# Kernel optimization log

Hardware: AMD Instinct MI355X
Metric: run time of the kernel (lower is better)

## Reference

```python
import jax, jax.numpy as jnp
import numpy as np
from functools import partial

H = 50  # hidden size hardcoded in the module


def _lstm_cell(x, h, c, W_ih, W_hh, b_ih, b_hh):
    # PyTorch LSTMCell math, gate order i, f, g, o
    gates = x @ W_ih.T + h @ W_hh.T + b_ih + b_hh  # [B, 4H]
    i, f, g, o = jnp.split(gates, 4, axis=-1)
    c_new = jax.nn.sigmoid(f) * c + jax.nn.sigmoid(i) * jnp.tanh(g)
    h_new = jax.nn.sigmoid(o) * jnp.tanh(c_new)
    return h_new, c_new


def setup_inputs() -> dict:
    key = jax.random.key(0)
    ks = jax.random.split(key, 11)
    B, T = 512, 1024

    def w(k, shape, fan_in):
        return (jax.random.normal(k, shape, jnp.float32) / np.sqrt(fan_in)).astype(jnp.float32)

    return {
        "x": jax.random.normal(ks[0], (B, T), jnp.float32),
        "W_ih1": w(ks[1], (4 * H, 1), H),
        "W_hh1": w(ks[2], (4 * H, H), H),
        "b_ih1": w(ks[3], (4 * H,), H),
        "b_hh1": w(ks[4], (4 * H,), H),
        "W_ih2": w(ks[5], (4 * H, H), H),
        "W_hh2": w(ks[6], (4 * H, H), H),
        "b_ih2": w(ks[7], (4 * H,), H),
        "b_hh2": w(ks[8], (4 * H,), H),
        "W_lin": w(ks[9], (1, H), H),
        "b_lin": w(ks[10], (1,), H),
        "predict": 32,
    }


def reference(x, W_ih1, W_hh1, b_ih1, b_hh1, W_ih2, W_hh2, b_ih2, b_hh2,
              W_lin, b_lin, predict):
    B = x.shape[0]
    z = jnp.zeros((B, H), x.dtype)
    init = (z, z, z, z)

    def step(carry, x_t):  # x_t: [B, 1]
        h1, c1, h2, c2 = carry
        h1, c1 = _lstm_cell(x_t, h1, c1, W_ih1, W_hh1, b_ih1, b_hh1)
        h2, c2 = _lstm_cell(h1, h2, c2, W_ih2, W_hh2, b_ih2, b_hh2)
        out = h2 @ W_lin.T + b_lin  # [B, 1]
        return (h1, c1, h2, c2), out

    xs = jnp.swapaxes(x, 0, 1)[:, :, None]  # [T, B, 1]
    carry, outs = jax.lax.scan(step, init, xs)  # outs: [T, B, 1]

    if predict > 0:
        h1, c1, h2, c2 = carry

        def pstep(pcarry, _):
            h1, c1, h2, c2, o = pcarry
            h1, c1 = _lstm_cell(o, h1, c1, W_ih1, W_hh1, b_ih1, b_hh1)
            h2, c2 = _lstm_cell(h1, h2, c2, W_ih2, W_hh2, b_ih2, b_hh2)
            out = h2 @ W_lin.T + b_lin
            return (h1, c1, h2, c2, out), out

        _, pouts = jax.lax.scan(pstep, (h1, c1, h2, c2, outs[-1]), None, length=predict)
        outs = jnp.concatenate([outs, pouts], axis=0)

    # stack(dim=1).squeeze(2) -> [B, T + predict]
    return jnp.swapaxes(outs[..., 0], 0, 1)
```

## Files before the change

### kernel.cpp

```cpp
#include <hip/hip_runtime.h>


#define Hh   50
#define TLEN 1024

typedef _Float16 half2v __attribute__((ext_vector_type(2)));

#if __has_builtin(__builtin_amdgcn_fdot2)
#define FDOT2(a, b, c) __builtin_amdgcn_fdot2((a), (b), (c), false)
#else
#define FDOT2(a, b, c) ((c) + (float)(a)[0] * (float)(b)[0] + (float)(a)[1] * (float)(b)[1])
#endif

#define BC(f) __builtin_bit_cast(half2v, f)

__device__ __forceinline__ float fast_sigmoid(float v) {
    return 1.0f / (1.0f + __expf(-v));
}
__device__ __forceinline__ float fast_tanh(float v) {
    return 1.0f - 2.0f / (__expf(2.0f * v) + 1.0f);
}
__device__ __forceinline__ void lds_fence() {
    asm volatile("" ::: "memory");
    __builtin_amdgcn_sched_barrier(0);
}

#define SHADOW(CARRY, BUF, SLOT) do {                                        \
    _Pragma("unroll")                                                        \
    for (int L_ = 0; L_ < 6; ++L_) {                                         \
        float4 f_ = *(const float4*)&BUF[SLOT][8 * L_];                      \
        CARRY[4*L_] = f_.x; CARRY[4*L_+1] = f_.y;                            \
        CARRY[4*L_+2] = f_.z; CARRY[4*L_+3] = f_.w;                          \
    }                                                                        \
    CARRY[24] = *(const float*)&BUF[SLOT][48];                               \
} while (0)

extern "C" __global__ __launch_bounds__(128, 1)
void sine_lstm_kernel(const float* __restrict__ x,
                      const float* __restrict__ W_ih1,
                      const float* __restrict__ W_hh1,
                      const float* __restrict__ b_ih1,
                      const float* __restrict__ b_hh1,
                      const float* __restrict__ W_ih2,
                      const float* __restrict__ W_hh2,
                      const float* __restrict__ b_ih2,
                      const float* __restrict__ b_hh2,
                      const float* __restrict__ W_lin,
                      const float* __restrict__ b_lin,
                      const int*   __restrict__ predict_p,
                      float* __restrict__ out,
                      int T)
{
    __shared__ __align__(16) float    x_lds[TLEN];
    __shared__ __align__(16) _Float16 h1lds[2][64];
    __shared__ __align__(16) _Float16 h2lds[2][64];
    __shared__ __align__(16) float    h2f32[2][64];
    __shared__ __align__(16) float    part[2][4][64][4];

    const int tid = threadIdx.x;
    const int wv  = tid >> 6;
    const int ln  = tid & 63;
    const bool isProd = (wv == 0);
    const int b   = blockIdx.x;
    const int predict = *predict_p;
    const int S = T + predict;

    for (int i = tid; i < TLEN; i += 128)
        x_lds[i] = x[(size_t)b * T + i];
    ((_Float16*)h1lds)[tid] = (_Float16)0.0f;
    ((_Float16*)h2lds)[tid] = (_Float16)0.0f;
    ((float*)h2f32)[tid] = 0.0f;

    const bool act = (ln < Hh);

    const float* MA = isProd ? W_hh1 : W_hh2;
    const int    pbase = isProd ? 0 : 12;
    half2v wgtA[4][25], wgtB[4][13];
    float  b1v[4], b2v[4], wih[4];
    #pragma unroll
    for (int q = 0; q < 4; ++q) {
        const int r = act ? (q * Hh + ln) : 0;
        b1v[q] = b_ih1[r] + b_hh1[r];
        b2v[q] = b_ih2[r] + b_hh2[r];
        wih[q] = W_ih1[r];
        #pragma unroll
        for (int p = 0; p < 25; ++p)
            wgtA[q][p] = half2v{(_Float16)MA[r * Hh + 2*p], (_Float16)MA[r * Hh + 2*p + 1]};
        #pragma unroll
        for (int p = 0; p < 13; ++p) {
            const int k0 = 2 * (pbase + p);
            wgtB[q][p] = half2v{(_Float16)W_ih2[r * Hh + k0], (_Float16)W_ih2[r * Hh + k0 + 1]};
        }
    }
    const float wlin_l = act ? W_lin[ln] : 0.0f;
    const float blin   = b_lin[0];

    float hc[25];
    #pragma unroll
    for (int p = 0; p < 25; ++p) hc[p] = 0.0f;
    float cst = 0.0f;

    __syncthreads();

    for (int t = 0; t <= S; ++t) {
        __syncthreads();
        const bool pred = (t >= T);

        if (!isProd && t >= 1) {
            const int sp = (t + 1) & 1;
            float acc[4][4];
            #pragma unroll
            for (int q = 0; q < 4; ++q) {
                float4 pr = *(const float4*)&part[sp][q][ln][0];
                acc[q][0] = pr.x; acc[q][1] = pr.y; acc[q][2] = pr.z; acc[q][3] = pr.w;
            }
            #pragma unroll
            for (int L = 3; L < 6; ++L) {
                float4 f = *(const float4*)&h1lds[sp][8 * L];
                #pragma unroll
                for (int j = 0; j < 4; ++j) {
                    const float hj = (&f.x)[j];
                    #pragma unroll
                    for (int q = 0; q < 4; ++q)
                        acc[q][j] = FDOT2(wgtB[q][4*(L-3) + j], BC(hj), acc[q][j]);
                }
            }
            {
                const float h24 = *(const float*)&h1lds[sp][48];
                #pragma unroll
                for (int q = 0; q < 4; ++q)
                    acc[q][0] = FDOT2(wgtB[q][12], BC(h24), acc[q][0]);
            }
            #pragma unroll
            for (int L = 0; L < 6; ++L) {
                #pragma unroll
                for (int j = 0; j < 4; ++j) {
                    const float hj = hc[4*L + j];
                    #pragma unroll
                    for (int q = 0; q < 4; ++q)
                        acc[q][j] = FDOT2(wgtA[q][4*L + j], BC(hj), acc[q][j]);
                }
            }
            #pragma unroll
            for (int q = 0; q < 4; ++q)
                acc[q][0] = FDOT2(wgtA[q][24], BC(hc[24]), acc[q][0]);
            float gi = (acc[0][0] + acc[0][2]) + (acc[0][1] + acc[0][3]);
            float gf = (acc[1][0] + acc[1][2]) + (acc[1][1] + acc[1][3]);
            float gg = (acc[2][0] + acc[2][2]) + (acc[2][1] + acc[2][3]);
            float go = (acc[3][0] + acc[3][2]) + (acc[3][1] + acc[3][3]);
            if (act) {
                float cn = fast_sigmoid(gf) * cst + fast_sigmoid(gi) * fast_tanh(gg);
                cst = cn;
                float hn = fast_sigmoid(go) * fast_tanh(cn);
                h2lds[(t + 1) & 1][ln] = (_Float16)hn;
                h2f32[(t + 1) & 1][ln] = hn;
            }
            lds_fence();
            SHADOW(hc, h2lds, (t + 1) & 1);
        }

        if (isProd && t >= 2 && t <= T) {
            float pt = act ? h2f32[t & 1][ln] * wlin_l : 0.0f;
            #pragma unroll
            for (int off = 32; off > 0; off >>= 1)
                pt += __shfl_down(pt, off);
            if (ln == 0) out[(size_t)b * S + (t - 2)] = pt + blin;
        }

        float xin = 0.0f;
        bool doG1 = false;
        if (!pred) {
            if (isProd) { xin = x_lds[t]; doG1 = true; }
        } else {
            __syncthreads();
            float pt = act ? h2f32[(t + 1) & 1][ln] * wlin_l : 0.0f;
            #pragma unroll
            for (int off = 32; off > 0; off >>= 1)
                pt += __shfl_down(pt, off);
            float o = __shfl(pt, 0) + blin;
            if (tid == 0) out[(size_t)b * S + (t - 1)] = o;
            if (isProd && t < S) { xin = o; doG1 = true; }
        }

        if (doG1) {
            float acc[4][4];
            #pragma unroll
            for (int q = 0; q < 4; ++q) {
                acc[q][0] = b1v[q] + xin * wih[q];
                acc[q][1] = 0.0f; acc[q][2] = 0.0f; acc[q][3] = 0.0f;
            }
            #pragma unroll
            for (int L = 0; L < 6; ++L) {
                #pragma unroll
                for (int j = 0; j < 4; ++j) {
                    const float hj = hc[4*L + j];
                    #pragma unroll
                    for (int q = 0; q < 4; ++q)
                        acc[q][j] = FDOT2(wgtA[q][4*L + j], BC(hj), acc[q][j]);
                }
            }
            #pragma unroll
            for (int q = 0; q < 4; ++q)
                acc[q][0] = FDOT2(wgtA[q][24], BC(hc[24]), acc[q][0]);
            float gi = (acc[0][0] + acc[0][2]) + (acc[0][1] + acc[0][3]);
            float gf = (acc[1][0] + acc[1][2]) + (acc[1][1] + acc[1][3]);
            float gg = (acc[2][0] + acc[2][2]) + (acc[2][1] + acc[2][3]);
            float go = (acc[3][0] + acc[3][2]) + (acc[3][1] + acc[3][3]);
            if (act) {
                float cn = fast_sigmoid(gf) * cst + fast_sigmoid(gi) * fast_tanh(gg);
                cst = cn;
                h1lds[t & 1][ln] = (_Float16)(fast_sigmoid(go) * fast_tanh(cn));
            }
            lds_fence();
            SHADOW(hc, h1lds, t & 1);
            float pa[4][4];
            #pragma unroll
            for (int q = 0; q < 4; ++q) {
                pa[q][0] = b2v[q]; pa[q][1] = 0.0f; pa[q][2] = 0.0f; pa[q][3] = 0.0f;
            }
            #pragma unroll
            for (int L = 0; L < 3; ++L) {
                #pragma unroll
                for (int j = 0; j < 4; ++j) {
                    const float hj = hc[4*L + j];
                    #pragma unroll
                    for (int q = 0; q < 4; ++q)
                        pa[q][j] = FDOT2(wgtB[q][4*L + j], BC(hj), pa[q][j]);
                }
            }
            #pragma unroll
            for (int q = 0; q < 4; ++q)
                *(float4*)&part[t & 1][q][ln][0] =
                    make_float4(pa[q][0], pa[q][1], pa[q][2], pa[q][3]);
        }
    }
}

extern "C" void kernel_launch(void* const* d_in, const int* in_sizes, int n_in,
                              void* d_out, int out_size, void* d_ws, size_t ws_size,
                              hipStream_t stream) {
    const float* x      = (const float*)d_in[0];
    const float* W_ih1  = (const float*)d_in[1];
    const float* W_hh1  = (const float*)d_in[2];
    const float* b_ih1  = (const float*)d_in[3];
    const float* b_hh1  = (const float*)d_in[4];
    const float* W_ih2  = (const float*)d_in[5];
    const float* W_hh2  = (const float*)d_in[6];
    const float* b_ih2  = (const float*)d_in[7];
    const float* b_hh2  = (const float*)d_in[8];
    const float* W_lin  = (const float*)d_in[9];
    const float* b_lin  = (const float*)d_in[10];
    const int*   pred   = (const int*)d_in[11];
    float* out = (float*)d_out;

    const int B = 512;
    const int T = in_sizes[0] / B;

    dim3 grid(B), block(128);
    hipLaunchKernelGGL(sine_lstm_kernel, grid, block, 0, stream,
                       x, W_ih1, W_hh1, b_ih1, b_hh1,
                       W_ih2, W_hh2, b_ih2, b_hh2,
                       W_lin, b_lin, pred, out, T);
}
```

Baseline: 1.148 ms.

## Rebalance two-wave LSTM pipeline so producer computes W_hh2 partial off critical path

Reassigns the work split between the two waves. The producer wave now holds W_hh1 plus half of W_hh2 and computes the layer-2 recurrent partial from h2 in parallel with its layer-1 gate matvec. The consumer wave holds W_ih2 plus the other half of W_hh2 and consumes h1 directly. A second barrier per step is added so the layer-1 activations and the layer-2 partial sums are exchanged at aligned points. This is meant to shorten the serial dependency chain per timestep, but it adds one extra __syncthreads per step and changes the part buffer to single-buffered.

```diff
diff --git a/kernel.cpp b/kernel.cpp
--- a/kernel.cpp
+++ b/kernel.cpp
@@ -55,7 +55,7 @@
     __shared__ __align__(16) _Float16 h1lds[2][64];
     __shared__ __align__(16) _Float16 h2lds[2][64];
     __shared__ __align__(16) float    h2f32[2][64];
-    __shared__ __align__(16) float    part[2][4][64][4];
+    __shared__ __align__(16) float    part[4][64][4];
 
     const int tid = threadIdx.x;
     const int wv  = tid >> 6;
@@ -73,8 +73,8 @@
 
     const bool act = (ln < Hh);
 
-    const float* MA = isProd ? W_hh1 : W_hh2;
-    const int    pbase = isProd ? 0 : 12;
+    const float* MA = isProd ? W_hh1 : W_ih2;
+    const int    pbase = isProd ? 12 : 0;
     half2v wgtA[4][25], wgtB[4][13];
     float  b1v[4], b2v[4], wih[4];
     #pragma unroll
@@ -89,7 +89,7 @@
         #pragma unroll
         for (int p = 0; p < 13; ++p) {
             const int k0 = 2 * (pbase + p);
-            wgtB[q][p] = half2v{(_Float16)W_ih2[r * Hh + k0], (_Float16)W_ih2[r * Hh + k0 + 1]};
+            wgtB[q][p] = half2v{(_Float16)W_hh2[r * Hh + k0], (_Float16)W_hh2[r * Hh + k0 + 1]};
         }
     }
     const float wlin_l = act ? W_lin[ln] : 0.0f;
@@ -99,6 +99,9 @@
     #pragma unroll
     for (int p = 0; p < 25; ++p) hc[p] = 0.0f;
     float cst = 0.0f;
+    float g1g[4];
+    #pragma unroll
+    for (int q = 0; q < 4; ++q) g1g[q] = 0.0f;
 
     __syncthreads();
 
@@ -106,48 +109,132 @@
         __syncthreads();
         const bool pred = (t >= T);
 
+        if (isProd) {
+            if (t >= 1) {
+                const int s2 = t & 1;
+                float pa[4][4];
+                #pragma unroll
+                for (int q = 0; q < 4; ++q) {
+                    pa[q][0] = 0.0f; pa[q][1] = 0.0f; pa[q][2] = 0.0f; pa[q][3] = 0.0f;
+                }
+                #pragma unroll
+                for (int L = 0; L < 3; ++L) {
+                    float4 f = *(const float4*)&h2lds[s2][8 * (3 + L)];
+                    #pragma unroll
+                    for (int j = 0; j < 4; ++j) {
+                        const float hj = (&f.x)[j];
+                        #pragma unroll
+                        for (int q = 0; q < 4; ++q)
+                            pa[q][j] = FDOT2(wgtB[q][4*L + j], BC(hj), pa[q][j]);
+                    }
+                }
+                {
+                    const float h24 = *(const float*)&h2lds[s2][48];
+                    #pragma unroll
+                    for (int q = 0; q < 4; ++q)
+                        pa[q][0] = FDOT2(wgtB[q][12], BC(h24), pa[q][0]);
+                }
+                #pragma unroll
+                for (int q = 0; q < 4; ++q)
+                    *(float4*)&part[q][ln][0] =
+                        make_float4(pa[q][0], pa[q][1], pa[q][2], pa[q][3]);
+            }
+            if (!pred) {
+                const float xin = x_lds[t];
+                float acc[4][4];
+                #pragma unroll
+                for (int q = 0; q < 4; ++q) {
+                    acc[q][0] = b1v[q] + xin * wih[q];
+                    acc[q][1] = 0.0f; acc[q][2] = 0.0f; acc[q][3] = 0.0f;
+                }
+                #pragma unroll
+                for (int L = 0; L < 6; ++L) {
+                    #pragma unroll
+                    for (int j = 0; j < 4; ++j) {
+                        const float hj = hc[4*L + j];
+                        #pragma unroll
+                        for (int q = 0; q < 4; ++q)
+                            acc[q][j] = FDOT2(wgtA[q][4*L + j], BC(hj), acc[q][j]);
+                    }
+                }
+                #pragma unroll
+                for (int q = 0; q < 4; ++q)
+                    acc[q][0] = FDOT2(wgtA[q][24], BC(hc[24]), acc[q][0]);
+                #pragma unroll
+                for (int q = 0; q < 4; ++q)
+                    g1g[q] = (acc[q][0] + acc[q][2]) + (acc[q][1] + acc[q][3]);
+            }
+        }
+        float cacc[4][4];
         if (!isProd && t >= 1) {
             const int sp = (t + 1) & 1;
-            float acc[4][4];
+            float4 f0 = *(const float4*)&h1lds[sp][0];
+            float4 f1 = *(const float4*)&h1lds[sp][8];
+            float4 f2 = *(const float4*)&h1lds[sp][16];
+            float4 f3 = *(const float4*)&h1lds[sp][24];
+            float4 f4 = *(const float4*)&h1lds[sp][32];
+            float4 f5 = *(const float4*)&h1lds[sp][40];
+            const float h24 = *(const float*)&h1lds[sp][48];
             #pragma unroll
             for (int q = 0; q < 4; ++q) {
-                float4 pr = *(const float4*)&part[sp][q][ln][0];
-                acc[q][0] = pr.x; acc[q][1] = pr.y; acc[q][2] = pr.z; acc[q][3] = pr.w;
-            }
-            #pragma unroll
-            for (int L = 3; L < 6; ++L) {
-                float4 f = *(const float4*)&h1lds[sp][8 * L];
-                #pragma unroll
-                for (int j = 0; j < 4; ++j) {
-                    const float hj = (&f.x)[j];
-                    #pragma unroll
-                    for (int q = 0; q < 4; ++q)
-                        acc[q][j] = FDOT2(wgtB[q][4*(L-3) + j], BC(hj), acc[q][j]);
-                }
-            }
-            {
-                const float h24 = *(const float*)&h1lds[sp][48];
-                #pragma unroll
-                for (int q = 0; q < 4; ++q)
-                    acc[q][0] = FDOT2(wgtB[q][12], BC(h24), acc[q][0]);
-            }
-            #pragma unroll
-            for (int L = 0; L < 6; ++L) {
+                cacc[q][0] = b2v[q]; cacc[q][1] = 0.0f; cacc[q][2] = 0.0f; cacc[q][3] = 0.0f;
+            }
+            #pragma unroll
+            for (int L = 0; L < 3; ++L) {
                 #pragma unroll
                 for (int j = 0; j < 4; ++j) {
                     const float hj = hc[4*L + j];
                     #pragma unroll
                     for (int q = 0; q < 4; ++q)
-                        acc[q][j] = FDOT2(wgtA[q][4*L + j], BC(hj), acc[q][j]);
+                        cacc[q][j] = FDOT2(wgtB[q][4*L + j], BC(hj), cacc[q][j]);
+                }
+            }
+            const float4* fs[6] = { &f0, &f1, &f2, &f3, &f4, &f5 };
+            #pragma unroll
+            for (int L = 0; L < 6; ++L) {
+                #pragma unroll
+                for (int j = 0; j < 4; ++j) {
+                    const float hj = (&fs[L]->x)[j];
+                    #pragma unroll
+                    for (int q = 0; q < 4; ++q)
+                        cacc[q][j] = FDOT2(wgtA[q][4*L + j], BC(hj), cacc[q][j]);
                 }
             }
             #pragma unroll
             for (int q = 0; q < 4; ++q)
-                acc[q][0] = FDOT2(wgtA[q][24], BC(hc[24]), acc[q][0]);
-            float gi = (acc[0][0] + acc[0][2]) + (acc[0][1] + acc[0][3]);
-            float gf = (acc[1][0] + acc[1][2]) + (acc[1][1] + acc[1][3]);
-            float gg = (acc[2][0] + acc[2][2]) + (acc[2][1] + acc[2][3]);
-            float go = (acc[3][0] + acc[3][2]) + (acc[3][1] + acc[3][3]);
+                cacc[q][0] = FDOT2(wgtA[q][24], BC(h24), cacc[q][0]);
+        }
+
+        __syncthreads();
+
+        if (isProd) {
+            if (!pred) {
+                float cn = fast_sigmoid(g1g[1]) * cst
+                         + fast_sigmoid(g1g[0]) * fast_tanh(g1g[2]);
+                cst = cn;
+                if (act) h1lds[t & 1][ln] =
+                    (_Float16)(fast_sigmoid(g1g[3]) * fast_tanh(cn));
+                lds_fence();
+                SHADOW(hc, h1lds, t & 1);
+            }
+            if (t >= 2 && t <= T) {
+                float pt = act ? h2f32[t & 1][ln] * wlin_l : 0.0f;
+                #pragma unroll
+                for (int off = 32; off > 0; off >>= 1)
+                    pt += __shfl_down(pt, off);
+                if (ln == 0) out[(size_t)b * S + (t - 2)] = pt + blin;
+            }
+        } else if (t >= 1) {
+            #pragma unroll
+            for (int q = 0; q < 4; ++q) {
+                float4 pr = *(const float4*)&part[q][ln][0];
+                cacc[q][0] += pr.x; cacc[q][1] += pr.y;
+                cacc[q][2] += pr.z; cacc[q][3] += pr.w;
+            }
+            float gi = (cacc[0][0] + cacc[0][2]) + (cacc[0][1] + cacc[0][3]);
+            float gf = (cacc[1][0] + cacc[1][2]) + (cacc[1][1] + cacc[1][3]);
+            float gg = (cacc[2][0] + cacc[2][2]) + (cacc[2][1] + cacc[2][3]);
+            float go = (cacc[3][0] + cacc[3][2]) + (cacc[3][1] + cacc[3][3]);
             if (act) {
                 float cn = fast_sigmoid(gf) * cst + fast_sigmoid(gi) * fast_tanh(gg);
                 cst = cn;
@@ -159,19 +246,7 @@
             SHADOW(hc, h2lds, (t + 1) & 1);
         }
 
-        if (isProd && t >= 2 && t <= T) {
-            float pt = act ? h2f32[t & 1][ln] * wlin_l : 0.0f;
-            #pragma unroll
-            for (int off = 32; off > 0; off >>= 1)
-                pt += __shfl_down(pt, off);
-            if (ln == 0) out[(size_t)b * S + (t - 2)] = pt + blin;
-        }
-
-        float xin = 0.0f;
-        bool doG1 = false;
-        if (!pred) {
-            if (isProd) { xin = x_lds[t]; doG1 = true; }
-        } else {
+        if (pred) {
             __syncthreads();
             float pt = act ? h2f32[(t + 1) & 1][ln] * wlin_l : 0.0f;
             #pragma unroll
@@ -179,59 +254,37 @@
                 pt += __shfl_down(pt, off);
             float o = __shfl(pt, 0) + blin;
             if (tid == 0) out[(size_t)b * S + (t - 1)] = o;
-            if (isProd && t < S) { xin = o; doG1 = true; }
-        }
-
-        if (doG1) {
-            float acc[4][4];
-            #pragma unroll
-            for (int q = 0; q < 4; ++q) {
-                acc[q][0] = b1v[q] + xin * wih[q];
-                acc[q][1] = 0.0f; acc[q][2] = 0.0f; acc[q][3] = 0.0f;
-            }
-            #pragma unroll
-            for (int L = 0; L < 6; ++L) {
-                #pragma unroll
-                for (int j = 0; j < 4; ++j) {
-                    const float hj = hc[4*L + j];
-                    #pragma unroll
-                    for (int q = 0; q < 4; ++q)
-                        acc[q][j] = FDOT2(wgtA[q][4*L + j], BC(hj), acc[q][j]);
-                }
-            }
-            #pragma unroll
-            for (int q = 0; q < 4; ++q)
-                acc[q][0] = FDOT2(wgtA[q][24], BC(hc[24]), acc[q][0]);
-            float gi = (acc[0][0] + acc[0][2]) + (acc[0][1] + acc[0][3]);
-            float gf = (acc[1][0] + acc[1][2]) + (acc[1][1] + acc[1][3]);
-            float gg = (acc[2][0] + acc[2][2]) + (acc[2][1] + acc[2][3]);
-            float go = (acc[3][0] + acc[3][2]) + (acc[3][1] + acc[3][3]);
-            if (act) {
+            if (isProd && t < S) {
+                float acc[4][4];
+                #pragma unroll
+                for (int q = 0; q < 4; ++q) {
+                    acc[q][0] = b1v[q] + o * wih[q];
+                    acc[q][1] = 0.0f; acc[q][2] = 0.0f; acc[q][3] = 0.0f;
+                }
+                #pragma unroll
+                for (int L = 0; L < 6; ++L) {
+                    #pragma unroll
+                    for (int j = 0; j < 4; ++j) {
+                        const float hj = hc[4*L + j];
+                        #pragma unroll
+                        for (int q = 0; q < 4; ++q)
+                            acc[q][j] = FDOT2(wgtA[q][4*L + j], BC(hj), acc[q][j]);
+                    }
+                }
+                #pragma unroll
+                for (int q = 0; q < 4; ++q)
+                    acc[q][0] = FDOT2(wgtA[q][24], BC(hc[24]), acc[q][0]);
+                float gi = (acc[0][0] + acc[0][2]) + (acc[0][1] + acc[0][3]);
+                float gf = (acc[1][0] + acc[1][2]) + (acc[1][1] + acc[1][3]);
+                float gg = (acc[2][0] + acc[2][2]) + (acc[2][1] + acc[2][3]);
+                float go = (acc[3][0] + acc[3][2]) + (acc[3][1] + acc[3][3]);
                 float cn = fast_sigmoid(gf) * cst + fast_sigmoid(gi) * fast_tanh(gg);
                 cst = cn;
-                h1lds[t & 1][ln] = (_Float16)(fast_sigmoid(go) * fast_tanh(cn));
-            }
-            lds_fence();
-            SHADOW(hc, h1lds, t & 1);
-            float pa[4][4];
-            #pragma unroll
-            for (int q = 0; q < 4; ++q) {
-                pa[q][0] = b2v[q]; pa[q][1] = 0.0f; pa[q][2] = 0.0f; pa[q][3] = 0.0f;
-            }
-            #pragma unroll
-            for (int L = 0; L < 3; ++L) {
-                #pragma unroll
-                for (int j = 0; j < 4; ++j) {
-                    const float hj = hc[4*L + j];
-                    #pragma unroll
-                    for (int q = 0; q < 4; ++q)
-                        pa[q][j] = FDOT2(wgtB[q][4*L + j], BC(hj), pa[q][j]);
-                }
-            }
-            #pragma unroll
-            for (int q = 0; q < 4; ++q)
-                *(float4*)&part[t & 1][q][ln][0] =
-                    make_float4(pa[q][0], pa[q][1], pa[q][2], pa[q][3]);
+                if (act) h1lds[t & 1][ln] =
+                    (_Float16)(fast_sigmoid(go) * fast_tanh(cn));
+                lds_fence();
+                SHADOW(hc, h1lds, t & 1);
+            }
         }
     }
 }
```

Measured after the change: 1.267 ms. +10.5%, slower.
